# Optimization experiments

Measured on AMD Instinct MI355X. Metric: run time of the kernel, lower is better.

The kernel has to match this reference:

```python
import jax, jax.numpy as jnp
import numpy as np

N, E, F_IN, H = 100000, 500000, 1433, 32


def setup_inputs() -> dict:
    key = jax.random.key(0)
    ks = jax.random.split(key, 8)
    return {
        "x": jax.random.normal(ks[0], (N, F_IN), jnp.float32),
        "edge_index": jax.random.randint(ks[1], (2, E), 0, N, dtype=jnp.int32),
        "W1l": jax.random.normal(ks[2], (H, F_IN), jnp.float32) * 0.02,
        "b1l": jnp.zeros((H,), jnp.float32),
        "W1r": jax.random.normal(ks[3], (H, F_IN), jnp.float32) * 0.02,
        "W2l": jax.random.normal(ks[4], (H, H), jnp.float32) * 0.1,
        "b2l": jnp.zeros((H,), jnp.float32),
        "W2r": jax.random.normal(ks[5], (H, H), jnp.float32) * 0.1,
    }


def _sage_conv(x, src, tgt, Wl, bl, Wr, n_nodes):
    # PyG SAGEConv (mean aggr): out = lin_l(mean_{j->i} x_j) + lin_r(x_i)
    msg_sum = jax.ops.segment_sum(x[src], tgt, num_segments=n_nodes)  # [N, d]
    cnt = jax.ops.segment_sum(jnp.ones((src.shape[0],), x.dtype), tgt,
                              num_segments=n_nodes)                  # [N]
    agg = msg_sum / jnp.maximum(cnt, 1.0)[:, None]  # isolated nodes -> 0
    return agg @ Wl.T + bl + x @ Wr.T


def reference(x, edge_index, W1l, b1l, W1r, W2l, b2l, W2r):
    src, tgt = edge_index[0], edge_index[1]
    n = x.shape[0]
    h = _sage_conv(x, src, tgt, W1l, b1l, W1r, n)   # [N, 32]
    h = _sage_conv(h, src, tgt, W2l, b2l, W2r, n)   # [N, 32]
    h = jax.nn.relu(h)
    # dropout is identity in eval mode (training=False)
    return jax.nn.log_softmax(h, axis=1)
```

## Files before the change

### kernel.cpp

```cpp
#include <hip/hip_runtime.h>
#include <hip/hip_bf16.h>


typedef __attribute__((ext_vector_type(8))) __bf16 bf16x8;
typedef __attribute__((ext_vector_type(4))) float f32x4;

constexpr int K1 = 1433;
constexpr int KP1 = 1536;
constexpr int BK = 32;
constexpr int NS = 45;
constexpr int BM = 128;

__device__ __forceinline__ void gload_lds16(const void* g, void* l) {
  __builtin_amdgcn_global_load_lds(
      reinterpret_cast<const __attribute__((address_space(1))) void*>(
          reinterpret_cast<uintptr_t>(g)),
      reinterpret_cast<__attribute__((address_space(3))) void*>(
          reinterpret_cast<uintptr_t>(l)),
      16, 0, 0);
}

__device__ __forceinline__ bf16x8 cvt8(const float4 lo, const float4 hi) {
  bf16x8 r;
  r[0] = (__bf16)lo.x; r[1] = (__bf16)lo.y;
  r[2] = (__bf16)lo.z; r[3] = (__bf16)lo.w;
  r[4] = (__bf16)hi.x; r[5] = (__bf16)hi.y;
  r[6] = (__bf16)hi.z; r[7] = (__bf16)hi.w;
  return r;
}

__global__ __launch_bounds__(256) void conv_w2(const float* __restrict__ W1l,
                                               const float* __restrict__ W1r,
                                               const float* __restrict__ W2l,
                                               const float* __restrict__ W2r,
                                               __bf16* __restrict__ wb1,
                                               __bf16* __restrict__ wb2) {
  const int t = blockIdx.x * 256 + threadIdx.x;
  if (t < 64 * KP1) {
    const int c = t / KP1, k = t - c * KP1;
    float v = 0.0f;
    if (k < K1)
      v = (c < 32) ? W1l[(long)c * K1 + k] : W1r[(long)(c - 32) * K1 + k];
    wb1[t] = (__bf16)v;
  } else {
    const int u = t - 64 * KP1;
    if (u < 64 * 32) {
      const int c = u >> 5, k = u & 31;
      const float v = (c < 32) ? W2l[c * 32 + k] : W2r[(c - 32) * 32 + k];
      wb2[u] = (__bf16)v;
    }
  }
}

__global__ __launch_bounds__(256) void gemm_big(const float* __restrict__ X,
                                                const __bf16* __restrict__ WB,
                                                float* __restrict__ Y,
                                                int Nrows) {
  __shared__ float ldsA[2][BM][BK];
  __shared__ __bf16 ldsB[2][64][BK];
  const int tid = threadIdx.x;
  const int w = tid >> 6, l = tid & 63;
  const int lr = l & 15, lg = l >> 4;
  const int row0 = blockIdx.x * BM;

  const int aRowIn = (l >> 3);
  const int aChunk = (l & 7) ^ aRowIn;
  long aRow[4];
#pragma unroll
  for (int i = 0; i < 4; ++i) {
    long r = (long)row0 + w * 32 + i * 8 + aRowIn;
    if (r >= Nrows) r = Nrows - 1;
    aRow[i] = r;
  }
  const float* const pAmax = X + (size_t)Nrows * K1 - 4;
  const int bRow = w * 16 + (l >> 2);
  const int bChunk = (l & 3) ^ ((l >> 3) & 3);
  const __bf16* const pB0 = WB + (long)bRow * KP1 + bChunk * 8;

  auto stage = [&](int s, int buf) {
    const int k0 = s * BK;
#pragma unroll
    for (int i = 0; i < 4; ++i) {
      const float* g = X + aRow[i] * K1 + k0 + aChunk * 4;
      if (g > pAmax) g = pAmax;
      gload_lds16(g, &ldsA[buf][w * 32 + i * 8][0]);
    }
    gload_lds16(pB0 + k0, &ldsB[buf][w * 16][0]);
  };

  f32x4 acc[2][4];
#pragma unroll
  for (int t = 0; t < 2; ++t)
#pragma unroll
    for (int j = 0; j < 4; ++j) acc[t][j] = (f32x4){0.f, 0.f, 0.f, 0.f};

  const int swzA = lr & 7;
  const int swzB = (lr >> 1) & 3;

  stage(0, 0);
#pragma unroll 1
  for (int s = 0; s < NS; ++s) {
    const int buf = s & 1;
    if (s + 1 < NS) {
      stage(s + 1, buf ^ 1);
      asm volatile("s_waitcnt vmcnt(5)" ::: "memory");
    } else {
      asm volatile("s_waitcnt vmcnt(0)" ::: "memory");
    }
    __builtin_amdgcn_s_barrier();
    __builtin_amdgcn_sched_barrier(0);
    bf16x8 bfrag[4];
#pragma unroll
    for (int ct = 0; ct < 4; ++ct) {
      const int br = ct * 16 + lr;
      bfrag[ct] = *reinterpret_cast<const bf16x8*>(
          &ldsB[buf][br][(lg ^ swzB) * 8]);
    }
#pragma unroll
    for (int t = 0; t < 2; ++t) {
      const int fr = w * 32 + t * 16 + lr;
      const float4 u = *reinterpret_cast<const float4*>(
          &ldsA[buf][fr][((lg * 2 + 0) ^ swzA) * 4]);
      const float4 v = *reinterpret_cast<const float4*>(
          &ldsA[buf][fr][((lg * 2 + 1) ^ swzA) * 4]);
      const bf16x8 af = cvt8(u, v);
#pragma unroll
      for (int ct = 0; ct < 4; ++ct)
        acc[t][ct] =
            __builtin_amdgcn_mfma_f32_16x16x32_bf16(af, bfrag[ct], acc[t][ct], 0, 0, 0);
    }
    __builtin_amdgcn_sched_barrier(0);
    __builtin_amdgcn_s_barrier();
  }

#pragma unroll
  for (int t = 0; t < 2; ++t) {
#pragma unroll
    for (int j = 0; j < 4; ++j) {
      const long R = (long)row0 + w * 32 + t * 16 + lg * 4 + j;
      if (R < Nrows) {
#pragma unroll
        for (int ct = 0; ct < 4; ++ct)
          Y[R * 64 + ct * 16 + lr] = acc[t][ct][j];
      }
    }
  }
}


__global__ __launch_bounds__(256) void hist_deg(const int* __restrict__ ei,
                                                int* __restrict__ deg, int E) {
  const int e = blockIdx.x * 256 + threadIdx.x;
  if (e < E) atomicAdd(&deg[ei[E + e]], 1);
}

__global__ __launch_bounds__(256) void scan_tilesum(const int* __restrict__ deg,
                                                    int* __restrict__ tileSum,
                                                    int n) {
  __shared__ int s[256];
  const int b = blockIdx.x, t = threadIdx.x;
  const int base = b * 2048 + t * 8;
  int v = 0;
#pragma unroll
  for (int j = 0; j < 8; ++j) {
    const int i = base + j;
    if (i < n) v += deg[i];
  }
  s[t] = v;
  __syncthreads();
  for (int d = 128; d > 0; d >>= 1) {
    if (t < d) s[t] += s[t + d];
    __syncthreads();
  }
  if (t == 0) tileSum[b] = s[0];
}

__global__ __launch_bounds__(256) void scan_offsets(const int* __restrict__ deg,
                                                    const int* __restrict__ tileSum,
                                                    int* __restrict__ off,
                                                    int n, int nT) {
  __shared__ int warpTot[4];
  __shared__ int tileOffS;
  const int b = blockIdx.x, t = threadIdx.x;
  if (t < 64) {
    int v = (t < b && t < nT) ? tileSum[t] : 0;
#pragma unroll
    for (int d = 1; d < 64; d <<= 1) v += __shfl_xor(v, d);
    if (t == 0) tileOffS = v;
  }
  const int base = b * 2048 + t * 8;
  int v[8];
  int s = 0;
#pragma unroll
  for (int j = 0; j < 8; ++j) {
    const int i = base + j;
    v[j] = (i < n) ? deg[i] : 0;
    s += v[j];
  }
  const int l = t & 63, w = t >> 6;
  int inc = s;
#pragma unroll
  for (int d = 1; d < 64; d <<= 1) {
    const int o = __shfl_up(inc, d);
    if (l >= d) inc += o;
  }
  if (l == 63) warpTot[w] = inc;
  __syncthreads();
  int wo = 0;
  for (int k = 0; k < w; ++k) wo += warpTot[k];
  int ex = wo + (inc - s) + tileOffS;
#pragma unroll
  for (int j = 0; j < 8; ++j) {
    const int i = base + j;
    if (i < n) {
      off[i] = ex;
      ex += v[j];
    }
  }
}

__global__ __launch_bounds__(256) void scatter_src(const int* __restrict__ ei,
                                                   const int* __restrict__ off,
                                                   int* __restrict__ fill,
                                                   int* __restrict__ ssrc,
                                                   int E) {
  const int e = blockIdx.x * 256 + threadIdx.x;
  if (e < E) {
    const int t = ei[E + e];
    const int p = off[t] + atomicAdd(&fill[t], 1);
    ssrc[p] = ei[e];
  }
}

__global__ __launch_bounds__(256) void agg_gemm2(
    const int* __restrict__ off, const int* __restrict__ deg,
    const int* __restrict__ ssrc, const float* __restrict__ Y,
    const float* __restrict__ b1, const __bf16* __restrict__ WB2,
    float* __restrict__ Y2, int N) {
  __shared__ __bf16 hs[64][40];
  const int tid = threadIdx.x;
  const int nb0 = blockIdx.x * 64;
  const int c = tid & 31, r8 = tid >> 5;

  int stA[8], dgA[8];
#pragma unroll
  for (int j = 0; j < 8; ++j) {
    const int i = nb0 + r8 * 8 + j;
    stA[j] = (i < N) ? off[i] : 0;
    dgA[j] = (i < N) ? deg[i] : 0;
  }
#pragma unroll 1
  for (int j = 0; j < 8; ++j) {
    const int i = nb0 + r8 * 8 + j;
    float hv = 0.0f;
    if (i < N) {
      const int st = stA[j], d = dgA[j];
      float acc = 0.0f;
      int e = 0;
      for (; e + 4 <= d; e += 4) {
        const int s0 = ssrc[st + e + 0];
        const int s1 = ssrc[st + e + 1];
        const int s2 = ssrc[st + e + 2];
        const int s3 = ssrc[st + e + 3];
        acc += Y[(long)s0 * 64 + c] + Y[(long)s1 * 64 + c] +
               Y[(long)s2 * 64 + c] + Y[(long)s3 * 64 + c];
      }
      for (; e < d; ++e) acc += Y[(long)ssrc[st + e] * 64 + c];
      hv = acc / fmaxf((float)d, 1.0f) + b1[c] + Y[(long)i * 64 + 32 + c];
    }
    hs[r8 * 8 + j][c] = (__bf16)hv;
  }
  __syncthreads();

  const int w = tid >> 6, l = tid & 63;
  const int lr = l & 15, lg = l >> 4;
  const bf16x8 af = *reinterpret_cast<const bf16x8*>(&hs[w * 16 + lr][lg * 8]);
  f32x4 acc4[4];
#pragma unroll
  for (int j = 0; j < 4; ++j) acc4[j] = (f32x4){0.f, 0.f, 0.f, 0.f};
#pragma unroll
  for (int ct = 0; ct < 4; ++ct) {
    const bf16x8 bf = *reinterpret_cast<const bf16x8*>(
        WB2 + (ct * 16 + lr) * 32 + lg * 8);
    acc4[ct] = __builtin_amdgcn_mfma_f32_16x16x32_bf16(af, bf, acc4[ct], 0, 0, 0);
  }
#pragma unroll
  for (int j = 0; j < 4; ++j) {
    const long R = (long)nb0 + w * 16 + lg * 4 + j;
    if (R < N) {
#pragma unroll
      for (int ct = 0; ct < 4; ++ct) Y2[R * 64 + ct * 16 + lr] = acc4[ct][j];
    }
  }
}

__global__ __launch_bounds__(256) void agg_final(
    const int* __restrict__ off, const int* __restrict__ deg,
    const int* __restrict__ ssrc, const float* __restrict__ Y,
    const float* __restrict__ bias, float* __restrict__ out, int N) {
  const int t = blockIdx.x * 256 + threadIdx.x;
  const int i = t >> 5, c = t & 31;
  if (i >= N) return;
  const int st = off[i], d = deg[i];
  float acc = 0.0f;
  int e = 0;
  for (; e + 4 <= d; e += 4) {
    const int s0 = ssrc[st + e + 0];
    const int s1 = ssrc[st + e + 1];
    const int s2 = ssrc[st + e + 2];
    const int s3 = ssrc[st + e + 3];
    acc += Y[(long)s0 * 64 + c] + Y[(long)s1 * 64 + c] +
           Y[(long)s2 * 64 + c] + Y[(long)s3 * 64 + c];
  }
  for (; e < d; ++e) acc += Y[(long)ssrc[st + e] * 64 + c];
  const float mean = acc / fmaxf((float)d, 1.0f);
  float v = mean + bias[c] + Y[(long)i * 64 + 32 + c];
  v = fmaxf(v, 0.0f);
  float m = v;
#pragma unroll
  for (int dd = 16; dd >= 1; dd >>= 1) m = fmaxf(m, __shfl_xor(m, dd));
  const float ex = __expf(v - m);
  float s = ex;
#pragma unroll
  for (int dd = 16; dd >= 1; dd >>= 1) s += __shfl_xor(s, dd);
  out[(long)i * 32 + c] = (v - m) - __logf(s);
}

extern "C" void kernel_launch(void* const* d_in, const int* in_sizes, int n_in,
                              void* d_out, int out_size, void* d_ws,
                              size_t ws_size, hipStream_t stream) {
  const float* x = (const float*)d_in[0];
  const int* ei = (const int*)d_in[1];
  const float* W1l = (const float*)d_in[2];
  const float* b1l = (const float*)d_in[3];
  const float* W1r = (const float*)d_in[4];
  const float* W2l = (const float*)d_in[5];
  const float* b2l = (const float*)d_in[6];
  const float* W2r = (const float*)d_in[7];
  float* out = (float*)d_out;

  const int N = in_sizes[0] / K1;
  const int E = in_sizes[1] / 2;
  const int nTiles = (N + 2047) / 2048;

  char* ws = (char*)d_ws;
  size_t o = 0;
  auto alloc = [&](size_t bytes) {
    void* p = ws + o;
    o += (bytes + 255) & ~(size_t)255;
    return p;
  };
  float* ycomb1 = (float*)alloc((size_t)N * 64 * 4);
  float* ycomb2 = (float*)alloc((size_t)N * 64 * 4);
  __bf16* wb1 = (__bf16*)alloc((size_t)64 * KP1 * 2);
  __bf16* wb2 = (__bf16*)alloc((size_t)64 * 32 * 2);
  int* deg = (int*)alloc((size_t)2 * N * 4);
  int* fill = deg + N;
  int* off = (int*)alloc((size_t)N * 4);
  int* ssrc = (int*)alloc((size_t)E * 4);
  int* tileSum = (int*)alloc(64 * 4);

  conv_w2<<<(64 * KP1 + 64 * 32 + 255) / 256, 256, 0, stream>>>(
      W1l, W1r, W2l, W2r, wb1, wb2);
  (void)hipMemsetAsync(deg, 0, (size_t)2 * N * 4, stream);
  hist_deg<<<(E + 255) / 256, 256, 0, stream>>>(ei, deg, E);
  scan_tilesum<<<nTiles, 256, 0, stream>>>(deg, tileSum, N);
  scan_offsets<<<nTiles, 256, 0, stream>>>(deg, tileSum, off, N, nTiles);
  scatter_src<<<(E + 255) / 256, 256, 0, stream>>>(ei, off, fill, ssrc, E);

  gemm_big<<<(N + BM - 1) / BM, 256, 0, stream>>>(x, wb1, ycomb1, N);
  agg_gemm2<<<(N + 63) / 64, 256, 0, stream>>>(off, deg, ssrc, ycomb1, b1l,
                                               wb2, ycomb2, N);
  agg_final<<<(N * 32 + 255) / 256, 256, 0, stream>>>(off, deg, ssrc, ycomb2,
                                                      b2l, out, N);
}
```

Baseline: 287.1 us.

## Halve GEMM row tile and deepen LDS pipeline to four stages

Reduces the big layer-1 GEMM block tile from 128 to 64 rows, so each wave computes one 16-row tile instead of two. The LDS ring grows from 2 to 4 buffers, loads are issued three stages ahead, and the trailing barrier per iteration is removed. The aim is more blocks in flight and better hiding of global-to-LDS load latency on this memory-bound fp32 read of X. The cost is more blocks overall and more B-matrix reloads per row, plus a subtler buffer-reuse ordering now that only one barrier guards each step.

```diff
diff --git a/kernel.cpp b/kernel.cpp
--- a/kernel.cpp
+++ b/kernel.cpp
@@ -9,7 +9,7 @@
 constexpr int KP1 = 1536;
 constexpr int BK = 32;
 constexpr int NS = 45;
-constexpr int BM = 128;
+constexpr int BM = 64;
 
 __device__ __forceinline__ void gload_lds16(const void* g, void* l) {
   __builtin_amdgcn_global_load_lds(
@@ -56,21 +56,21 @@
                                                 const __bf16* __restrict__ WB,
                                                 float* __restrict__ Y,
                                                 int Nrows) {
-  __shared__ float ldsA[2][BM][BK];
-  __shared__ __bf16 ldsB[2][64][BK];
+  __shared__ float ldsA[4][BM][BK];
+  __shared__ __bf16 ldsB[4][64][BK];
   const int tid = threadIdx.x;
   const int w = tid >> 6, l = tid & 63;
   const int lr = l & 15, lg = l >> 4;
   const int row0 = blockIdx.x * BM;
 
-  const int aRowIn = (l >> 3);
+  const int aRowIn = l >> 3;
   const int aChunk = (l & 7) ^ aRowIn;
-  long aRow[4];
-#pragma unroll
-  for (int i = 0; i < 4; ++i) {
-    long r = (long)row0 + w * 32 + i * 8 + aRowIn;
+  long aRowG[2];
+#pragma unroll
+  for (int i = 0; i < 2; ++i) {
+    long r = (long)row0 + w * 16 + i * 8 + aRowIn;
     if (r >= Nrows) r = Nrows - 1;
-    aRow[i] = r;
+    aRowG[i] = r;
   }
   const float* const pAmax = X + (size_t)Nrows * K1 - 4;
   const int bRow = w * 16 + (l >> 2);
@@ -80,69 +80,65 @@
   auto stage = [&](int s, int buf) {
     const int k0 = s * BK;
 #pragma unroll
-    for (int i = 0; i < 4; ++i) {
-      const float* g = X + aRow[i] * K1 + k0 + aChunk * 4;
+    for (int i = 0; i < 2; ++i) {
+      const float* g = X + aRowG[i] * K1 + k0 + aChunk * 4;
       if (g > pAmax) g = pAmax;
-      gload_lds16(g, &ldsA[buf][w * 32 + i * 8][0]);
+      gload_lds16(g, &ldsA[buf][w * 16 + i * 8][0]);
     }
     gload_lds16(pB0 + k0, &ldsB[buf][w * 16][0]);
   };
 
-  f32x4 acc[2][4];
-#pragma unroll
-  for (int t = 0; t < 2; ++t)
-#pragma unroll
-    for (int j = 0; j < 4; ++j) acc[t][j] = (f32x4){0.f, 0.f, 0.f, 0.f};
+  f32x4 acc[4];
+#pragma unroll
+  for (int ct = 0; ct < 4; ++ct) acc[ct] = (f32x4){0.f, 0.f, 0.f, 0.f};
 
   const int swzA = lr & 7;
   const int swzB = (lr >> 1) & 3;
 
   stage(0, 0);
+  stage(1, 1);
+  stage(2, 2);
+  int bufC = 0;
 #pragma unroll 1
   for (int s = 0; s < NS; ++s) {
-    const int buf = s & 1;
-    if (s + 1 < NS) {
-      stage(s + 1, buf ^ 1);
-      asm volatile("s_waitcnt vmcnt(5)" ::: "memory");
+    if (s < NS - 2) {
+      asm volatile("s_waitcnt vmcnt(6)" ::: "memory");
+    } else if (s == NS - 2) {
+      asm volatile("s_waitcnt vmcnt(3)" ::: "memory");
     } else {
       asm volatile("s_waitcnt vmcnt(0)" ::: "memory");
     }
     __builtin_amdgcn_s_barrier();
     __builtin_amdgcn_sched_barrier(0);
+    if (s + 3 < NS) stage(s + 3, (bufC + 3) & 3);
     bf16x8 bfrag[4];
 #pragma unroll
     for (int ct = 0; ct < 4; ++ct) {
-      const int br = ct * 16 + lr;
       bfrag[ct] = *reinterpret_cast<const bf16x8*>(
-          &ldsB[buf][br][(lg ^ swzB) * 8]);
-    }
-#pragma unroll
-    for (int t = 0; t < 2; ++t) {
-      const int fr = w * 32 + t * 16 + lr;
+          &ldsB[bufC][ct * 16 + lr][(lg ^ swzB) * 8]);
+    }
+    {
+      const char* arow = (const char*)&ldsA[bufC][w * 16 + lr][0];
       const float4 u = *reinterpret_cast<const float4*>(
-          &ldsA[buf][fr][((lg * 2 + 0) ^ swzA) * 4]);
+          arow + (((lg * 2 + 0) ^ swzA) * 16));
       const float4 v = *reinterpret_cast<const float4*>(
-          &ldsA[buf][fr][((lg * 2 + 1) ^ swzA) * 4]);
+          arow + (((lg * 2 + 1) ^ swzA) * 16));
       const bf16x8 af = cvt8(u, v);
 #pragma unroll
       for (int ct = 0; ct < 4; ++ct)
-        acc[t][ct] =
-            __builtin_amdgcn_mfma_f32_16x16x32_bf16(af, bfrag[ct], acc[t][ct], 0, 0, 0);
+        acc[ct] =
+            __builtin_amdgcn_mfma_f32_16x16x32_bf16(af, bfrag[ct], acc[ct], 0, 0, 0);
     }
     __builtin_amdgcn_sched_barrier(0);
-    __builtin_amdgcn_s_barrier();
-  }
-
-#pragma unroll
-  for (int t = 0; t < 2; ++t) {
-#pragma unroll
-    for (int j = 0; j < 4; ++j) {
-      const long R = (long)row0 + w * 32 + t * 16 + lg * 4 + j;
-      if (R < Nrows) {
-#pragma unroll
-        for (int ct = 0; ct < 4; ++ct)
-          Y[R * 64 + ct * 16 + lr] = acc[t][ct][j];
-      }
+    bufC = (bufC + 1) & 3;
+  }
+
+#pragma unroll
+  for (int j = 0; j < 4; ++j) {
+    const long R = (long)row0 + w * 16 + lg * 4 + j;
+    if (R < Nrows) {
+#pragma unroll
+      for (int ct = 0; ct < 4; ++ct) Y[R * 64 + ct * 16 + lr] = acc[ct][j];
     }
   }
 }
```

New measurement: 302.5 us. 1.05x slower.
